# Kernel tuning notes

Measured on AMD Instinct MI355X. Metric: run time of the kernel, lower is better.

## Reference

```python
import jax, jax.numpy as jnp
import numpy as np

B, N, NV, P, S, H, DE, DO, NCLS = 128, 64, 14, 32, 14, 128, 64, 64, 5


def _edge_indices(n):
    # all ordered pairs (r, s), r != s — same order as itertools.product with diagonal removed
    idx = np.array([(r, s) for r in range(n) for s in range(n) if r != s], dtype=np.int32)
    return jnp.asarray(idx[:, 0]), jnp.asarray(idx[:, 1])


def _lin(key, fin, fout):
    kw, kb = jax.random.split(key)
    lim = 1.0 / np.sqrt(fin)
    w = jax.random.uniform(kw, (fin, fout), jnp.float32, -lim, lim)
    b = jax.random.uniform(kb, (fout,), jnp.float32, -lim, lim)
    return w, b


def _mlp3(h, w1, b1, w2, b2, w3, b3):
    h = jax.nn.relu(h @ w1 + b1)
    h = jax.nn.relu(h @ w2 + b2)
    return jax.nn.relu(h @ w3 + b3)


def setup_inputs() -> dict:
    key = jax.random.key(0)
    ks = jax.random.split(key, 12)
    inp = {
        'x': jax.random.normal(ks[0], (B, P, N), jnp.float32),
        'y': jax.random.normal(ks[1], (B, S, NV), jnp.float32),
    }
    inp['fr1_w'], inp['fr1_b'] = _lin(ks[2], 2 * P, H)
    inp['fr2_w'], inp['fr2_b'] = _lin(ks[3], H, H)
    inp['fr3_w'], inp['fr3_b'] = _lin(ks[4], H, DE)
    inp['fr1pv_w'], inp['fr1pv_b'] = _lin(ks[5], P + S, H)
    inp['fr2pv_w'], inp['fr2pv_b'] = _lin(ks[6], H, H)
    inp['fr3pv_w'], inp['fr3pv_b'] = _lin(ks[7], H, DE)
    inp['fo1_w'], inp['fo1_b'] = _lin(ks[8], P + 2 * DE, H)
    inp['fo2_w'], inp['fo2_b'] = _lin(ks[9], H, H)
    inp['fo3_w'], inp['fo3_b'] = _lin(ks[10], H, DO)
    inp['fc_w'], inp['fc_b'] = _lin(ks[11], DO, NCLS)
    return inp


def reference(x, y, fr1_w, fr1_b, fr2_w, fr2_b, fr3_w, fr3_b,
              fr1pv_w, fr1pv_b, fr2pv_w, fr2pv_b, fr3pv_w, fr3pv_b,
              fo1_w, fo1_b, fo2_w, fo2_b, fo3_w, fo3_b, fc_w, fc_b):
    b, p, n = x.shape
    nv = y.shape[2]
    de = fr3_w.shape[1]
    xT = jnp.transpose(x, (0, 2, 1))  # [B, N, P]
    yT = jnp.transpose(y, (0, 2, 1))  # [B, Nv, S]

    # particle-particle edges: one-hot Rr/Rs matmuls == gather by (receiver, sender)
    r_idx, s_idx = _edge_indices(n)
    epp_in = jnp.concatenate([xT[:, r_idx], xT[:, s_idx]], axis=-1)  # [B, Nr, 2P]
    E_pp = _mlp3(epp_in, fr1_w, fr1_b, fr2_w, fr2_b, fr3_w, fr3_b)   # [B, Nr, De]
    # E @ Rr^T == scatter-add onto receivers
    Ebar_pp = jnp.zeros((b, n, de), x.dtype).at[:, r_idx].add(E_pp)  # [B, N, De]

    # particle-vertex edges: Rk/Rv one-hot gathers over product(N, Nv)
    k_idx = jnp.repeat(jnp.arange(n), nv)
    v_idx = jnp.tile(jnp.arange(nv), n)
    epv_in = jnp.concatenate([xT[:, k_idx], yT[:, v_idx]], axis=-1)  # [B, Nt, P+S]
    E_pv = _mlp3(epv_in, fr1pv_w, fr1pv_b, fr2pv_w, fr2pv_b, fr3pv_w, fr3pv_b)
    Ebar_pv = jnp.zeros((b, n, de), x.dtype).at[:, k_idx].add(E_pv)  # [B, N, De]
    # (the torch code also computes Ebar_vp = E @ Rv^T but never uses it)

    C = jnp.concatenate([xT, Ebar_pp, Ebar_pv], axis=-1)  # [B, N, P+2De]
    O = _mlp3(C, fo1_w, fo1_b, fo2_w, fo2_b, fo3_w, fo3_b)  # [B, N, Do]
    pooled = jnp.sum(O, axis=1)  # [B, Do]
    return pooled @ fc_w + fc_b  # [B, n_targets]
```

## Files before the change

### kernel.cpp

```cpp
#include <hip/hip_runtime.h>

typedef __attribute__((ext_vector_type(8))) _Float16 half8;
typedef __attribute__((ext_vector_type(4))) _Float16 half4v;
typedef __attribute__((ext_vector_type(4))) float floatx4;

#define NB 128
#define NN 64
#define NV 14
#define PP 32
#define SS 14
#define HH 128
#define DE 64
#define NCLS 5
#define PITCH 136

#define OFF_W2   0
#define OFF_W3   16384
#define OFF_W2PV 24576
#define OFF_W3PV 40960
#define OFF_FO1  49152
#define OFF_FO2  69632
#define OFF_FO3  86016

__device__ __forceinline__ floatx4 MFMA(half8 a, half8 b, floatx4 c) {
  return __builtin_amdgcn_mfma_f32_16x16x32_f16(a, b, c, 0, 0, 0);
}

__global__ __launch_bounds__(256) void k0_prep(
    const float* __restrict__ x, const float* __restrict__ y,
    const float* __restrict__ fr1_w, const float* __restrict__ fr1_b,
    const float* __restrict__ fr1pv_w, const float* __restrict__ fr1pv_b,
    const float* __restrict__ fr2_w, const float* __restrict__ fr3_w,
    const float* __restrict__ fr2pv_w, const float* __restrict__ fr3pv_w,
    const float* __restrict__ fo1_w, const float* __restrict__ fo2_w,
    const float* __restrict__ fo3_w,
    _Float16* __restrict__ A1h, _Float16* __restrict__ B1h,
    _Float16* __restrict__ A1pvh, _Float16* __restrict__ B1pvh,
    _Float16* __restrict__ WT, float* __restrict__ dout) {
  int blk = blockIdx.x;
  int tid = threadIdx.x;
  if (blk < 768) {
    int mat = blk >> 8, sub = blk & 255;
    int b = sub >> 1, n0 = (sub & 1) << 5;
    __shared__ float sxT[32 * 33];
    for (int i = tid; i < 32 * PP; i += 256) {
      int p = i >> 5, n = i & 31;
      sxT[n * 33 + p] = x[b * (PP * NN) + p * 64 + n0 + n];
    }
    __syncthreads();
    const float* w; _Float16* outp; const float* bias;
    if (mat == 0)      { w = fr1_w;           outp = A1h;   bias = fr1_b; }
    else if (mat == 1) { w = fr1_w + 32 * HH; outp = B1h;   bias = nullptr; }
    else               { w = fr1pv_w;         outp = A1pvh; bias = fr1pv_b; }
    for (int o = tid; o < 32 * 32; o += 256) {
      int n = o >> 5, jc = o & 31;
      float4 acc = {0.f, 0.f, 0.f, 0.f};
      const float* xr = &sxT[n * 33];
#pragma unroll 8
      for (int k = 0; k < PP; k++) {
        float xv = xr[k];
        float4 wv = ((const float4*)w)[k * 32 + jc];
        acc.x += xv * wv.x; acc.y += xv * wv.y;
        acc.z += xv * wv.z; acc.w += xv * wv.w;
      }
      if (bias) {
        float4 bv = ((const float4*)bias)[jc];
        acc.x += bv.x; acc.y += bv.y; acc.z += bv.z; acc.w += bv.w;
      }
      half4v hv;
      hv[0] = (_Float16)acc.x; hv[1] = (_Float16)acc.y;
      hv[2] = (_Float16)acc.z; hv[3] = (_Float16)acc.w;
      *(half4v*)(&outp[(b * NN + n0 + n) * HH + jc * 4]) = hv;
    }
  } else if (blk < 896) {
    int b = blk - 768;
    __shared__ float syT[NV * 15];
    for (int i = tid; i < SS * NV; i += 256) {
      int s = i / NV, v = i - s * NV;
      syT[v * 15 + s] = y[b * (SS * NV) + i];
    }
    __syncthreads();
    const float4* w4 = (const float4*)(fr1pv_w + 32 * HH);
    for (int o = tid; o < NV * 32; o += 256) {
      int v = o >> 5, jc = o & 31;
      float4 acc = {0.f, 0.f, 0.f, 0.f};
#pragma unroll
      for (int s = 0; s < SS; s++) {
        float yv = syT[v * 15 + s];
        float4 wv = w4[s * 32 + jc];
        acc.x += yv * wv.x; acc.y += yv * wv.y;
        acc.z += yv * wv.z; acc.w += yv * wv.w;
      }
      half4v hv;
      hv[0] = (_Float16)acc.x; hv[1] = (_Float16)acc.y;
      hv[2] = (_Float16)acc.z; hv[3] = (_Float16)acc.w;
      *(half4v*)(&B1pvh[(b * NV + v) * HH + jc * 4]) = hv;
    }
  } else if (blk < 925) {
    int t = blk - 896;
    int wid, ks;
    if (t < 16)      { wid = t >> 2; ks = t & 3; }
    else if (t < 21) { wid = 4; ks = t - 16; }
    else if (t < 25) { wid = 5; ks = t - 21; }
    else             { wid = 6; ks = t - 25; }
    const float* src; int N, NKS, NTN; _Float16* dst;
    switch (wid) {
      case 0: src = fr2_w;   N = 128; NKS = 4; NTN = 8; dst = WT + OFF_W2;   break;
      case 1: src = fr3_w;   N = 64;  NKS = 4; NTN = 4; dst = WT + OFF_W3;   break;
      case 2: src = fr2pv_w; N = 128; NKS = 4; NTN = 8; dst = WT + OFF_W2PV; break;
      case 3: src = fr3pv_w; N = 64;  NKS = 4; NTN = 4; dst = WT + OFF_W3PV; break;
      case 4: src = fo1_w;   N = 128; NKS = 5; NTN = 8; dst = WT + OFF_FO1;  break;
      case 5: src = fo2_w;   N = 128; NKS = 4; NTN = 8; dst = WT + OFF_FO2;  break;
      default: src = fo3_w;  N = 64;  NKS = 4; NTN = 4; dst = WT + OFF_FO3;  break;
    }
    __shared__ float sw[32 * 132];
    int NP = N + 4;
    int n4 = N >> 2;
    for (int i = tid; i < 32 * n4; i += 256) {
      int row = i / n4, c4 = i - row * n4;
      *(float4*)(&sw[row * NP + c4 * 4]) = *(const float4*)(&src[(ks * 32 + row) * N + c4 * 4]);
    }
    __syncthreads();
    for (int o = tid; o < NTN * 64; o += 256) {
      int nt = o >> 6, l = o & 63;
      int cc = l & 15, qq = l >> 4;
      half8 hv;
#pragma unroll
      for (int j = 0; j < 8; j++) hv[j] = (_Float16)sw[(qq * 8 + j) * NP + nt * 16 + cc];
      *(half8*)(&dst[((nt * NKS + ks) * 64 + l) << 3]) = hv;
    }
  } else {
    for (int i = tid; i < NB * NCLS; i += 256) dout[i] = 0.f;
  }
}

__device__ __forceinline__ void pp_wave(
    const _Float16* __restrict__ Arow, const _Float16* __restrict__ Bb,
    const _Float16* sW2, const _Float16* __restrict__ w3g,
    const float* sB2, const float* sB3,
    _Float16* sH, int r, int lane, float* __restrict__ outp) {
  int c = lane & 15, q = lane >> 4;
  half8 av[4];
#pragma unroll
  for (int ks = 0; ks < 4; ks++)
    av[ks] = *(const half8*)(Arow + ks * 32 + q * 8);
  floatx4 regS = {0.f, 0.f, 0.f, 0.f};
#pragma unroll 1
  for (int tp = 0; tp < 2; tp++) {
    int z0 = 0;
    asm volatile("" : "+v"(z0));
    int tb0 = tp * 32, tb1 = tb0 + 16;
    int jj0 = tb0 + c; if (jj0 > 62) jj0 = 62;
    int s0 = jj0 + (jj0 >= r ? 1 : 0);
    int jj1 = tb1 + c; if (jj1 > 62) jj1 = 62;
    int s1 = jj1 + (jj1 >= r ? 1 : 0);
    const _Float16* b0p = Bb + s0 * HH;
    const _Float16* b1p = Bb + s1 * HH;
    floatx4 acc0[8], acc1[8];
#pragma unroll
    for (int nt = 0; nt < 8; nt++) {
      acc0[nt] = (floatx4){0.f, 0.f, 0.f, 0.f};
      acc1[nt] = (floatx4){0.f, 0.f, 0.f, 0.f};
    }
#pragma unroll
    for (int ks = 0; ks < 4; ks++) {
      half8 bv0 = *(const half8*)(b0p + ks * 32 + q * 8);
      half8 bv1 = *(const half8*)(b1p + ks * 32 + q * 8);
      half8 h0 = av[ks] + bv0;
      half8 h1 = av[ks] + bv1;
#pragma unroll
      for (int j = 0; j < 8; j++) {
        h0[j] = h0[j] > (_Float16)0.f ? h0[j] : (_Float16)0.f;
        h1[j] = h1[j] > (_Float16)0.f ? h1[j] : (_Float16)0.f;
      }
#pragma unroll
      for (int nt = 0; nt < 8; nt++) {
        half8 w = *(const half8*)(&sW2[z0 + ((nt * 4 + ks) << 9) + (lane << 3)]);
        acc0[nt] = MFMA(w, h0, acc0[nt]);
        acc1[nt] = MFMA(w, h1, acc1[nt]);
      }
    }
    half4v g1r[8];
#pragma unroll
    for (int nt = 0; nt < 8; nt++) {
      float4 bbt = *(const float4*)(&sB2[z0 + nt * 16 + q * 4]);
      half4v g0, g1;
      g0[0] = (_Float16)fmaxf(acc0[nt][0] + bbt.x, 0.f);
      g0[1] = (_Float16)fmaxf(acc0[nt][1] + bbt.y, 0.f);
      g0[2] = (_Float16)fmaxf(acc0[nt][2] + bbt.z, 0.f);
      g0[3] = (_Float16)fmaxf(acc0[nt][3] + bbt.w, 0.f);
      g1[0] = (_Float16)fmaxf(acc1[nt][0] + bbt.x, 0.f);
      g1[1] = (_Float16)fmaxf(acc1[nt][1] + bbt.y, 0.f);
      g1[2] = (_Float16)fmaxf(acc1[nt][2] + bbt.z, 0.f);
      g1[3] = (_Float16)fmaxf(acc1[nt][3] + bbt.w, 0.f);
      int slot = ((nt << 1) + (q >> 1)) ^ c;
      int addr = (c << 7) + (slot << 3) + ((q & 1) << 2);
      *(half4v*)(&sH[addr]) = g0;
      g1r[nt] = g1;
    }
    half8 a20[4], a21[4];
#pragma unroll
    for (int ks = 0; ks < 4; ks++) {
      int addr = (c << 7) + ((((ks << 2) + q) ^ c) << 3);
      a20[ks] = *(const half8*)(&sH[addr]);
    }
#pragma unroll
    for (int nt = 0; nt < 8; nt++) {
      int slot = ((nt << 1) + (q >> 1)) ^ c;
      int addr = (c << 7) + (slot << 3) + ((q & 1) << 2);
      *(half4v*)(&sH[addr]) = g1r[nt];
    }
#pragma unroll
    for (int ks = 0; ks < 4; ks++) {
      int addr = (c << 7) + ((((ks << 2) + q) ^ c) << 3);
      a21[ks] = *(const half8*)(&sH[addr]);
    }
#pragma unroll
    for (int nt3 = 0; nt3 < 4; nt3++) {
      floatx4 e0 = {0.f, 0.f, 0.f, 0.f};
      floatx4 e1 = {0.f, 0.f, 0.f, 0.f};
#pragma unroll
      for (int ks = 0; ks < 4; ks++) {
        half8 wf = *(const half8*)(&w3g[z0 + ((nt3 * 4 + ks) << 9) + (lane << 3)]);
        e0 = MFMA(a20[ks], wf, e0);
        e1 = MFMA(a21[ks], wf, e1);
      }
      float b3v = sB3[z0 + nt3 * 16 + c];
      int rb0 = tb0 + q * 4, rb1 = tb1 + q * 4;
#pragma unroll
      for (int rg = 0; rg < 4; rg++) {
        if (rb0 + rg < 63) regS[nt3] += fmaxf(e0[rg] + b3v, 0.f);
        if (rb1 + rg < 63) regS[nt3] += fmaxf(e1[rg] + b3v, 0.f);
      }
    }
  }
  float t0 = regS[0], t1 = regS[1], t2 = regS[2], t3 = regS[3];
  t0 += __shfl_xor(t0, 16); t0 += __shfl_xor(t0, 32);
  t1 += __shfl_xor(t1, 16); t1 += __shfl_xor(t1, 32);
  t2 += __shfl_xor(t2, 16); t2 += __shfl_xor(t2, 32);
  t3 += __shfl_xor(t3, 16); t3 += __shfl_xor(t3, 32);
  float v = q == 0 ? t0 : (q == 1 ? t1 : (q == 2 ? t2 : t3));
  outp[q * 16 + c] = v;
}

__device__ __forceinline__ void pv_wave(
    const _Float16* __restrict__ Arow, const _Float16* __restrict__ Bb,
    const _Float16* sW2, const _Float16* __restrict__ w3g,
    const float* sB2, const float* sB3,
    _Float16* sH, int lane, float* __restrict__ outp) {
  int c = lane & 15, q = lane >> 4;
  int z0 = 0;
  asm volatile("" : "+v"(z0));
  int v14 = c > 13 ? 13 : c;
  const _Float16* bp = Bb + v14 * HH;
  half8 av[4];
#pragma unroll
  for (int ks = 0; ks < 4; ks++)
    av[ks] = *(const half8*)(Arow + ks * 32 + q * 8);
  floatx4 acc[8];
#pragma unroll
  for (int nt = 0; nt < 8; nt++) acc[nt] = (floatx4){0.f, 0.f, 0.f, 0.f};
#pragma unroll
  for (int ks = 0; ks < 4; ks++) {
    half8 bv = *(const half8*)(bp + ks * 32 + q * 8);
    half8 h = av[ks] + bv;
#pragma unroll
    for (int j = 0; j < 8; j++) h[j] = h[j] > (_Float16)0.f ? h[j] : (_Float16)0.f;
#pragma unroll
    for (int nt = 0; nt < 8; nt++) {
      half8 w = *(const half8*)(&sW2[z0 + ((nt * 4 + ks) << 9) + (lane << 3)]);
      acc[nt] = MFMA(w, h, acc[nt]);
    }
  }
#pragma unroll
  for (int nt = 0; nt < 8; nt++) {
    float4 bbt = *(const float4*)(&sB2[z0 + nt * 16 + q * 4]);
    half4v g0;
    g0[0] = (_Float16)fmaxf(acc[nt][0] + bbt.x, 0.f);
    g0[1] = (_Float16)fmaxf(acc[nt][1] + bbt.y, 0.f);
    g0[2] = (_Float16)fmaxf(acc[nt][2] + bbt.z, 0.f);
    g0[3] = (_Float16)fmaxf(acc[nt][3] + bbt.w, 0.f);
    int slot = ((nt << 1) + (q >> 1)) ^ c;
    int addr = (c << 7) + (slot << 3) + ((q & 1) << 2);
    *(half4v*)(&sH[addr]) = g0;
  }
  half8 a2[4];
#pragma unroll
  for (int ks = 0; ks < 4; ks++) {
    int addr = (c << 7) + ((((ks << 2) + q) ^ c) << 3);
    a2[ks] = *(const half8*)(&sH[addr]);
  }
  floatx4 regS = {0.f, 0.f, 0.f, 0.f};
#pragma unroll
  for (int nt3 = 0; nt3 < 4; nt3++) {
    floatx4 e = {0.f, 0.f, 0.f, 0.f};
#pragma unroll
    for (int ks = 0; ks < 4; ks++) {
      half8 wf = *(const half8*)(&w3g[z0 + ((nt3 * 4 + ks) << 9) + (lane << 3)]);
      e = MFMA(a2[ks], wf, e);
    }
    float b3v = sB3[z0 + nt3 * 16 + c];
    int rb = q * 4;
#pragma unroll
    for (int rg = 0; rg < 4; rg++) {
      if (rb + rg < 14) regS[nt3] += fmaxf(e[rg] + b3v, 0.f);
    }
  }
  float t0 = regS[0], t1 = regS[1], t2 = regS[2], t3 = regS[3];
  t0 += __shfl_xor(t0, 16); t0 += __shfl_xor(t0, 32);
  t1 += __shfl_xor(t1, 16); t1 += __shfl_xor(t1, 32);
  t2 += __shfl_xor(t2, 16); t2 += __shfl_xor(t2, 32);
  t3 += __shfl_xor(t3, 16); t3 += __shfl_xor(t3, 32);
  float v = q == 0 ? t0 : (q == 1 ? t1 : (q == 2 ? t2 : t3));
  outp[q * 16 + c] = v;
}

#define PPB3 (NB * 4)
#define EGRID3 (NB * 4 + NB * 2)
__global__ __launch_bounds__(256, 2) void edge_fused(
    const _Float16* __restrict__ A1h, const _Float16* __restrict__ B1h,
    const _Float16* __restrict__ A1pvh, const _Float16* __restrict__ B1pvh,
    const float* __restrict__ fr2_b, const float* __restrict__ fr3_b,
    const float* __restrict__ fr2pv_b, const float* __restrict__ fr3pv_b,
    const _Float16* __restrict__ WT,
    float* __restrict__ Epp, float* __restrict__ Epv) {
  __shared__ __align__(16) _Float16 sW2[16384];
  __shared__ __align__(16) _Float16 sH2s[4][2048];
  __shared__ __align__(16) float sB2[128];
  __shared__ __align__(16) float sB3[64];
  int tid = threadIdx.x;
  int lane = tid & 63, wv = tid >> 6;
  bool ispp = blockIdx.x < PPB3;
  const _Float16* w2src = ispp ? (WT + OFF_W2) : (WT + OFF_W2PV);
  for (int i = tid; i < 2048; i += 256)
    *(uint4*)(&sW2[i * 8]) = *(const uint4*)(&w2src[i * 8]);
  const float* b2g = ispp ? fr2_b : fr2pv_b;
  const float* b3g = ispp ? fr3_b : fr3pv_b;
  if (tid < 128) sB2[tid] = b2g[tid];
  else if (tid < 192) sB3[tid - 128] = b3g[tid - 128];
  __syncthreads();
  if (ispp) {
    int b = blockIdx.x >> 2, r0 = (blockIdx.x & 3) << 4;
#pragma unroll 1
    for (int rcv = 0; rcv < 4; rcv++) {
      int r = r0 + wv * 4 + rcv;
      pp_wave(A1h + (b * NN + r) * HH, B1h + b * NN * HH,
              sW2, WT + OFF_W3, sB2, sB3,
              &sH2s[wv][0], r, lane, Epp + (b * NN + r) * DE);
    }
  } else {
    int p = blockIdx.x - PPB3;
    int b = p >> 1, hf2 = p & 1;
#pragma unroll 1
    for (int kk = 0; kk < 8; kk++) {
      int k = hf2 * 32 + wv * 8 + kk;
      pv_wave(A1pvh + (b * NN + k) * HH, B1pvh + b * NV * HH,
              sW2, WT + OFF_W3PV, sB2, sB3,
              &sH2s[wv][0], lane, Epv + (b * NN + k) * DE);
    }
  }
}

__global__ __launch_bounds__(256) void node_out(
    const float* __restrict__ x, const float* __restrict__ Epp,
    const float* __restrict__ Epv,
    const float* __restrict__ fo1_b, const float* __restrict__ fo2_b,
    const float* __restrict__ fo3_b,
    const float* __restrict__ fc_w, const float* __restrict__ fc_b,
    const _Float16* __restrict__ WT, float* __restrict__ out) {
  __shared__ _Float16 sC[16 * 168];
  __shared__ _Float16 sHa[16 * PITCH];
  __shared__ _Float16 sHb[16 * PITCH];
  __shared__ float sPool[64];
  int tid = threadIdx.x;
  int b = blockIdx.x >> 2, r0 = (blockIdx.x & 3) << 4;
  for (int i = tid; i < 16 * 32; i += 256) {
    int row = i >> 5, p = i & 31;
    sC[row * 168 + p] = (_Float16)x[b * (PP * NN) + p * 64 + r0 + row];
  }
  for (int i = tid; i < 16 * 16; i += 256) {
    int row = i >> 4, d4 = i & 15;
    float4 vpp = *(const float4*)(&Epp[(b * NN + r0 + row) * DE + d4 * 4]);
    float4 vpv = *(const float4*)(&Epv[(b * NN + r0 + row) * DE + d4 * 4]);
    half4v hpp, hpv;
    hpp[0] = (_Float16)vpp.x; hpp[1] = (_Float16)vpp.y;
    hpp[2] = (_Float16)vpp.z; hpp[3] = (_Float16)vpp.w;
    hpv[0] = (_Float16)vpv.x; hpv[1] = (_Float16)vpv.y;
    hpv[2] = (_Float16)vpv.z; hpv[3] = (_Float16)vpv.w;
    *(half4v*)(&sC[row * 168 + 32 + d4 * 4]) = hpp;
    *(half4v*)(&sC[row * 168 + 96 + d4 * 4]) = hpv;
  }
  __syncthreads();
  int lane = tid & 63, wv = tid >> 6;
  int c = lane & 15, q = lane >> 4;
  half8 cf[5];
#pragma unroll
  for (int ks = 0; ks < 5; ks++)
    cf[ks] = *(const half8*)(&sC[c * 168 + ks * 32 + q * 8]);
#pragma unroll
  for (int nt2 = 0; nt2 < 2; nt2++) {
    int nt = wv * 2 + nt2;
    floatx4 a0 = {0.f, 0.f, 0.f, 0.f};
#pragma unroll
    for (int ks = 0; ks < 5; ks++) {
      half8 wf = *(const half8*)(&WT[OFF_FO1 + ((nt * 5 + ks) << 9) + (lane << 3)]);
      a0 = MFMA(wf, cf[ks], a0);
    }
    float4 bb = *(const float4*)(&fo1_b[nt * 16 + q * 4]);
    half4v h0;
    h0[0] = (_Float16)fmaxf(a0[0] + bb.x, 0.f);
    h0[1] = (_Float16)fmaxf(a0[1] + bb.y, 0.f);
    h0[2] = (_Float16)fmaxf(a0[2] + bb.z, 0.f);
    h0[3] = (_Float16)fmaxf(a0[3] + bb.w, 0.f);
    *(half4v*)(&sHa[c * PITCH + nt * 16 + q * 4]) = h0;
  }
  __syncthreads();
  half8 g1[4];
#pragma unroll
  for (int ks = 0; ks < 4; ks++)
    g1[ks] = *(const half8*)(&sHa[c * PITCH + ks * 32 + q * 8]);
#pragma unroll
  for (int nt2 = 0; nt2 < 2; nt2++) {
    int nt = wv * 2 + nt2;
    floatx4 a0 = {0.f, 0.f, 0.f, 0.f};
#pragma unroll
    for (int ks = 0; ks < 4; ks++) {
      half8 wf = *(const half8*)(&WT[OFF_FO2 + ((nt * 4 + ks) << 9) + (lane << 3)]);
      a0 = MFMA(wf, g1[ks], a0);
    }
    float4 bb = *(const float4*)(&fo2_b[nt * 16 + q * 4]);
    half4v h0;
    h0[0] = (_Float16)fmaxf(a0[0] + bb.x, 0.f);
    h0[1] = (_Float16)fmaxf(a0[1] + bb.y, 0.f);
    h0[2] = (_Float16)fmaxf(a0[2] + bb.z, 0.f);
    h0[3] = (_Float16)fmaxf(a0[3] + bb.w, 0.f);
    *(half4v*)(&sHb[c * PITCH + nt * 16 + q * 4]) = h0;
  }
  __syncthreads();
  half8 g2[4];
#pragma unroll
  for (int ks = 0; ks < 4; ks++)
    g2[ks] = *(const half8*)(&sHb[c * PITCH + ks * 32 + q * 8]);
  floatx4 e0 = {0.f, 0.f, 0.f, 0.f};
#pragma unroll
  for (int ks = 0; ks < 4; ks++) {
    half8 wf = *(const half8*)(&WT[OFF_FO3 + ((wv * 4 + ks) << 9) + (lane << 3)]);
    e0 = MFMA(g2[ks], wf, e0);
  }
  float bb3 = fo3_b[wv * 16 + c];
  float s = 0.f;
#pragma unroll
  for (int rg = 0; rg < 4; rg++) s += fmaxf(e0[rg] + bb3, 0.f);
  s += __shfl_xor(s, 16);
  s += __shfl_xor(s, 32);
  if (lane < 16) sPool[wv * 16 + c] = s;
  __syncthreads();
  if (tid < NCLS) {
    float o = ((blockIdx.x & 3) == 0) ? fc_b[tid] : 0.f;
#pragma unroll
    for (int d = 0; d < 64; d++) o += sPool[d] * fc_w[d * NCLS + tid];
    atomicAdd(&out[b * NCLS + tid], o);
  }
}

extern "C" void kernel_launch(void* const* d_in, const int* in_sizes, int n_in,
                              void* d_out, int out_size, void* d_ws, size_t ws_size,
                              hipStream_t stream) {
  const float* x = (const float*)d_in[0];
  const float* y = (const float*)d_in[1];
  const float* fr1_w = (const float*)d_in[2];  const float* fr1_b = (const float*)d_in[3];
  const float* fr2_w = (const float*)d_in[4];  const float* fr2_b = (const float*)d_in[5];
  const float* fr3_w = (const float*)d_in[6];  const float* fr3_b = (const float*)d_in[7];
  const float* fr1pv_w = (const float*)d_in[8];  const float* fr1pv_b = (const float*)d_in[9];
  const float* fr2pv_w = (const float*)d_in[10]; const float* fr2pv_b = (const float*)d_in[11];
  const float* fr3pv_w = (const float*)d_in[12]; const float* fr3pv_b = (const float*)d_in[13];
  const float* fo1_w = (const float*)d_in[14];  const float* fo1_b = (const float*)d_in[15];
  const float* fo2_w = (const float*)d_in[16];  const float* fo2_b = (const float*)d_in[17];
  const float* fo3_w = (const float*)d_in[18];  const float* fo3_b = (const float*)d_in[19];
  const float* fc_w = (const float*)d_in[20];   const float* fc_b = (const float*)d_in[21];

  char* ws = (char*)d_ws;
  _Float16* A1h   = (_Float16*)(ws);
  _Float16* B1h   = (_Float16*)(ws + (2u << 20));
  _Float16* A1pvh = (_Float16*)(ws + (4u << 20));
  _Float16* B1pvh = (_Float16*)(ws + (6u << 20));
  _Float16* WT    = (_Float16*)(ws + (7u << 20));
  float* Epp      = (float*)(ws + (8u << 20));
  float* Epv      = (float*)(ws + (10u << 20));

  k0_prep<<<926, 256, 0, stream>>>(x, y, fr1_w, fr1_b, fr1pv_w, fr1pv_b,
                                   fr2_w, fr3_w, fr2pv_w, fr3pv_w,
                                   fo1_w, fo2_w, fo3_w,
                                   A1h, B1h, A1pvh, B1pvh, WT, (float*)d_out);
  edge_fused<<<EGRID3, 256, 0, stream>>>(A1h, B1h, A1pvh, B1pvh,
                                         fr2_b, fr3_b, fr2pv_b, fr3pv_b,
                                         WT, Epp, Epv);
  node_out<<<NB * 4, 256, 0, stream>>>(x, Epp, Epv, fo1_b, fo2_b, fo3_b,
                                       fc_w, fc_b, WT, (float*)d_out);
}
```

Measured before the change: 165.2 us.

## Halve edge kernel LDS weight staging and double pp block count for occupancy

The edge kernel now stages only the first half of the W2 weight tiles in shared memory and reads the other half plus the biases directly from global memory (L1/L2 cached). This cuts LDS use per block so launch bounds can request 4 blocks per CU instead of 2. Particle-particle blocks now cover 8 receivers each instead of 16, doubling the pp grid and shortening the per-block weight-load prologue relative to the work. The cost is more global/cache traffic for the weight fragments inside the inner MFMA loop, and tighter register limits from the higher occupancy target.

New measurement: 213.6 us. +29.2%, slower.

```diff
diff --git a/kernel.cpp b/kernel.cpp
--- a/kernel.cpp
+++ b/kernel.cpp
@@ -136,8 +136,9 @@
 
 __device__ __forceinline__ void pp_wave(
     const _Float16* __restrict__ Arow, const _Float16* __restrict__ Bb,
-    const _Float16* sW2, const _Float16* __restrict__ w3g,
-    const float* sB2, const float* sB3,
+    const _Float16* sW2, const _Float16* __restrict__ w2g,
+    const _Float16* __restrict__ w3g,
+    const float* __restrict__ b2g, const float* __restrict__ b3g,
     _Float16* sH, int r, int lane, float* __restrict__ outp) {
   int c = lane & 15, q = lane >> 4;
   half8 av[4];
@@ -175,7 +176,9 @@
       }
 #pragma unroll
       for (int nt = 0; nt < 8; nt++) {
-        half8 w = *(const half8*)(&sW2[z0 + ((nt * 4 + ks) << 9) + (lane << 3)]);
+        half8 w;
+        if (nt < 4) w = *(const half8*)(&sW2[((nt * 4 + ks) << 9) + (lane << 3)]);
+        else        w = *(const half8*)(&w2g[z0 + ((nt * 4 + ks) << 9) + (lane << 3)]);
         acc0[nt] = MFMA(w, h0, acc0[nt]);
         acc1[nt] = MFMA(w, h1, acc1[nt]);
       }
@@ -183,7 +186,7 @@
     half4v g1r[8];
 #pragma unroll
     for (int nt = 0; nt < 8; nt++) {
-      float4 bbt = *(const float4*)(&sB2[z0 + nt * 16 + q * 4]);
+      float4 bbt = *(const float4*)(&b2g[z0 + nt * 16 + q * 4]);
       half4v g0, g1;
       g0[0] = (_Float16)fmaxf(acc0[nt][0] + bbt.x, 0.f);
       g0[1] = (_Float16)fmaxf(acc0[nt][1] + bbt.y, 0.f);
@@ -225,7 +228,7 @@
         e0 = MFMA(a20[ks], wf, e0);
         e1 = MFMA(a21[ks], wf, e1);
       }
-      float b3v = sB3[z0 + nt3 * 16 + c];
+      float b3v = b3g[z0 + nt3 * 16 + c];
       int rb0 = tb0 + q * 4, rb1 = tb1 + q * 4;
 #pragma unroll
       for (int rg = 0; rg < 4; rg++) {
@@ -245,8 +248,9 @@
 
 __device__ __forceinline__ void pv_wave(
     const _Float16* __restrict__ Arow, const _Float16* __restrict__ Bb,
-    const _Float16* sW2, const _Float16* __restrict__ w3g,
-    const float* sB2, const float* sB3,
+    const _Float16* sW2, const _Float16* __restrict__ w2g,
+    const _Float16* __restrict__ w3g,
+    const float* __restrict__ b2g, const float* __restrict__ b3g,
     _Float16* sH, int lane, float* __restrict__ outp) {
   int c = lane & 15, q = lane >> 4;
   int z0 = 0;
@@ -268,13 +272,15 @@
     for (int j = 0; j < 8; j++) h[j] = h[j] > (_Float16)0.f ? h[j] : (_Float16)0.f;
 #pragma unroll
     for (int nt = 0; nt < 8; nt++) {
-      half8 w = *(const half8*)(&sW2[z0 + ((nt * 4 + ks) << 9) + (lane << 3)]);
+      half8 w;
+      if (nt < 4) w = *(const half8*)(&sW2[((nt * 4 + ks) << 9) + (lane << 3)]);
+      else        w = *(const half8*)(&w2g[z0 + ((nt * 4 + ks) << 9) + (lane << 3)]);
       acc[nt] = MFMA(w, h, acc[nt]);
     }
   }
 #pragma unroll
   for (int nt = 0; nt < 8; nt++) {
-    float4 bbt = *(const float4*)(&sB2[z0 + nt * 16 + q * 4]);
+    float4 bbt = *(const float4*)(&b2g[z0 + nt * 16 + q * 4]);
     half4v g0;
     g0[0] = (_Float16)fmaxf(acc[nt][0] + bbt.x, 0.f);
     g0[1] = (_Float16)fmaxf(acc[nt][1] + bbt.y, 0.f);
@@ -299,7 +305,7 @@
       half8 wf = *(const half8*)(&w3g[z0 + ((nt3 * 4 + ks) << 9) + (lane << 3)]);
       e = MFMA(a2[ks], wf, e);
     }
-    float b3v = sB3[z0 + nt3 * 16 + c];
+    float b3v = b3g[z0 + nt3 * 16 + c];
     int rb = q * 4;
 #pragma unroll
     for (int rg = 0; rg < 4; rg++) {
@@ -315,47 +321,43 @@
   outp[q * 16 + c] = v;
 }
 
-#define PPB3 (NB * 4)
-#define EGRID3 (NB * 4 + NB * 2)
-__global__ __launch_bounds__(256, 2) void edge_fused(
+#define PPB4 (NB * 8)
+#define EGRID4 (NB * 8 + NB * 2)
+__global__ __launch_bounds__(256, 4) void edge_fused(
     const _Float16* __restrict__ A1h, const _Float16* __restrict__ B1h,
     const _Float16* __restrict__ A1pvh, const _Float16* __restrict__ B1pvh,
     const float* __restrict__ fr2_b, const float* __restrict__ fr3_b,
     const float* __restrict__ fr2pv_b, const float* __restrict__ fr3pv_b,
     const _Float16* __restrict__ WT,
     float* __restrict__ Epp, float* __restrict__ Epv) {
-  __shared__ __align__(16) _Float16 sW2[16384];
+  __shared__ __align__(16) _Float16 sW2[8192];
   __shared__ __align__(16) _Float16 sH2s[4][2048];
-  __shared__ __align__(16) float sB2[128];
-  __shared__ __align__(16) float sB3[64];
   int tid = threadIdx.x;
   int lane = tid & 63, wv = tid >> 6;
-  bool ispp = blockIdx.x < PPB3;
-  const _Float16* w2src = ispp ? (WT + OFF_W2) : (WT + OFF_W2PV);
-  for (int i = tid; i < 2048; i += 256)
-    *(uint4*)(&sW2[i * 8]) = *(const uint4*)(&w2src[i * 8]);
+  bool ispp = blockIdx.x < PPB4;
+  const _Float16* w2base = ispp ? (WT + OFF_W2) : (WT + OFF_W2PV);
+  for (int i = tid; i < 1024; i += 256)
+    *(uint4*)(&sW2[i * 8]) = *(const uint4*)(&w2base[i * 8]);
   const float* b2g = ispp ? fr2_b : fr2pv_b;
   const float* b3g = ispp ? fr3_b : fr3pv_b;
-  if (tid < 128) sB2[tid] = b2g[tid];
-  else if (tid < 192) sB3[tid - 128] = b3g[tid - 128];
   __syncthreads();
   if (ispp) {
-    int b = blockIdx.x >> 2, r0 = (blockIdx.x & 3) << 4;
+    int b = blockIdx.x >> 3, rb = (blockIdx.x & 7) << 3;
 #pragma unroll 1
-    for (int rcv = 0; rcv < 4; rcv++) {
-      int r = r0 + wv * 4 + rcv;
+    for (int rcv = 0; rcv < 2; rcv++) {
+      int r = rb + wv * 2 + rcv;
       pp_wave(A1h + (b * NN + r) * HH, B1h + b * NN * HH,
-              sW2, WT + OFF_W3, sB2, sB3,
+              sW2, WT + OFF_W2, WT + OFF_W3, b2g, b3g,
               &sH2s[wv][0], r, lane, Epp + (b * NN + r) * DE);
     }
   } else {
-    int p = blockIdx.x - PPB3;
-    int b = p >> 1, hf2 = p & 1;
+    int p = blockIdx.x - PPB4;
+    int b = p >> 1, k0 = (p & 1) << 5;
 #pragma unroll 1
     for (int kk = 0; kk < 8; kk++) {
-      int k = hf2 * 32 + wv * 8 + kk;
+      int k = k0 + wv * 8 + kk;
       pv_wave(A1pvh + (b * NN + k) * HH, B1pvh + b * NV * HH,
-              sW2, WT + OFF_W3PV, sB2, sB3,
+              sW2, WT + OFF_W2PV, WT + OFF_W3PV, b2g, b3g,
               &sH2s[wv][0], lane, Epv + (b * NN + k) * DE);
     }
   }
@@ -492,7 +494,7 @@
                                    fr2_w, fr3_w, fr2pv_w, fr3pv_w,
                                    fo1_w, fo2_w, fo3_w,
                                    A1h, B1h, A1pvh, B1pvh, WT, (float*)d_out);
-  edge_fused<<<EGRID3, 256, 0, stream>>>(A1h, B1h, A1pvh, B1pvh,
+  edge_fused<<<EGRID4, 256, 0, stream>>>(A1h, B1h, A1pvh, B1pvh,
                                          fr2_b, fr3_b, fr2pv_b, fr3pv_b,
                                          WT, Epp, Epv);
   node_out<<<NB * 4, 256, 0, stream>>>(x, Epp, Epv, fo1_b, fo2_b, fo3_b,
```
